# Performance work log

Measured on AMD Instinct MI355X. Metric: run time of the kernel, lower is better.

The kernel has to match this reference:

```python
import jax, jax.numpy as jnp
import numpy as np

B, A, D = 512, 32, 256      # batch clips, actors (nodes per graph), feature dim
E = 1048576                 # total edges over the flattened (B*A)-node graph
THRESHOLD = 0.5             # config.knn.threshold
EPS = 1e-5


def setup_inputs() -> dict:
    key = jax.random.key(0)
    k1, k2, k3 = jax.random.split(key, 3)
    N = B * A
    X = jax.random.normal(k1, (B, A, D), dtype=jnp.float32)
    edge_index = jax.random.randint(k2, (2, E), 0, N, dtype=jnp.int32)
    W = jax.random.normal(k3, (D, D), dtype=jnp.float32) * (1.0 / np.sqrt(D))
    b = jnp.zeros((D,), dtype=jnp.float32)
    return {"X": X, "edge_index": edge_index, "W": W, "b": b}


def gcn_conv(x, edge_index, W, b):
    # Standard GCNConv: x' = D^-1/2 (A + I) D^-1/2 (x W) + b
    N = x.shape[0]
    x = x @ W                                            # [N, D]
    loop = jnp.arange(N, dtype=edge_index.dtype)
    src = jnp.concatenate([edge_index[0], loop])         # message sources
    tgt = jnp.concatenate([edge_index[1], loop])         # aggregation targets
    deg = jax.ops.segment_sum(jnp.ones_like(src, dtype=x.dtype), tgt,
                              num_segments=N)            # in-degree incl. self-loop
    dinv = jnp.where(deg > 0, jax.lax.rsqrt(deg), 0.0)
    coef = (dinv[src] * dinv[tgt])[:, None]              # symmetric norm per edge
    out = jax.ops.segment_sum(x[src] * coef, tgt, num_segments=N)
    return out + b


def reference(X, edge_index, W, b):
    Bq, Aq, Dq = X.shape
    x = X.reshape(Bq * Aq, Dq)
    x = gcn_conv(x, edge_index, W, b)
    Xo = x.reshape(Bq, Aq, Dq)

    # cal_edge: pairwise squared distances per batch, min-max normalized,
    # thresholded. Instead of variable-length dense_to_sparse edge lists we
    # return the equivalent fixed-shape adjacency mask [B, A, A].
    inner = -2.0 * jnp.einsum('bad,bcd->bac', Xo, Xo)
    sq = jnp.sum(Xo * Xo, axis=-1, keepdims=True)        # [B, A, 1]
    scores = sq + inner + jnp.swapaxes(sq, -1, -2)       # [B, A, A]
    smin = scores.min(axis=-1, keepdims=True)
    smax = scores.max(axis=-1, keepdims=True)
    scores = (scores - smin) / (smax - smin + EPS)
    adj_mask = scores > THRESHOLD                        # new edge set (dense form)
    return Xo, adj_mask
```

## Files before the change

kernel.cpp:

```cpp
#include <hip/hip_runtime.h>

#define BQ 512
#define AQ 32
#define DQ 256
#define NQ (BQ * AQ)
#define EQ 1048576
#define THR 0.5f
#define EPSF 1e-5f
#define DEG_STRIDE 160
#define BIN_TGTS 64
#define NBINS (NQ / BIN_TGTS)
#define NBLK_P 256
#define EPB (EQ / NBLK_P)

typedef __attribute__((ext_vector_type(8))) short bf16x8;
typedef __attribute__((ext_vector_type(4))) float f32x4;

__device__ __forceinline__ unsigned short f2bf(float f) {
    unsigned int u = __float_as_uint(f);
    return (unsigned short)((u + 0x7FFFu + ((u >> 16) & 1u)) >> 16);
}
__device__ __forceinline__ float bf2f(unsigned short h) {
    return __uint_as_float((unsigned int)h << 16);
}

__global__ __launch_bounds__(256) void k_wt_part(
        const float* __restrict__ W, unsigned short* __restrict__ Wt,
        const int* __restrict__ src, const int* __restrict__ tgt,
        int* __restrict__ cntT, int* __restrict__ offT,
        unsigned int* __restrict__ binned) {
    __shared__ unsigned int buf[EPB];
    __shared__ int hist[NBINS];
    __shared__ int sdat[NBINS];
    __shared__ int cur[NBINS];
    int tid = threadIdx.x;
    if (blockIdx.x < 256) {
        int idx = blockIdx.x * 256 + tid;
        int n = idx >> 8;
        int k = idx & 255;
        float w = W[k * DQ + n];
        unsigned short h = f2bf(w);
        Wt[idx] = h;
        Wt[DQ * DQ + idx] = f2bf(w - bf2f(h));
        return;
    }
    int blk = blockIdx.x - 256;
    hist[tid] = 0;
    __syncthreads();
    int base = blk * EPB;
    int t[16], s[16];
    #pragma unroll
    for (int i = 0; i < 16; i++) {
        int e = base + i * 256 + tid;
        t[i] = tgt[e];
        s[i] = src[e];
        atomicAdd(&hist[t[i] >> 6], 1);
    }
    __syncthreads();
    int v = hist[tid];
    sdat[tid] = v;
    __syncthreads();
    #pragma unroll
    for (int off = 1; off < 256; off <<= 1) {
        int add = (tid >= off) ? sdat[tid - off] : 0;
        __syncthreads();
        sdat[tid] += add;
        __syncthreads();
    }
    int excl = sdat[tid] - v;
    cur[tid] = excl;
    cntT[blk * NBINS + tid] = v;
    offT[blk * NBINS + tid] = excl;
    __syncthreads();
    #pragma unroll
    for (int i = 0; i < 16; i++) {
        int pos = atomicAdd(&cur[t[i] >> 6], 1);
        buf[pos] = ((unsigned int)t[i] << 14) | (unsigned int)s[i];
    }
    __syncthreads();
    unsigned int* g = binned + (size_t)blk * EPB;
    #pragma unroll
    for (int i = 0; i < 16; i++) g[i * 256 + tid] = buf[i * 256 + tid];
}

__global__ __launch_bounds__(256) void k_gemm_cnt(
        const float* __restrict__ Xp, const unsigned short* __restrict__ Wt,
        unsigned short* __restrict__ xwb,
        const int* __restrict__ cntT, const int* __restrict__ offT,
        const unsigned int* __restrict__ binned,
        float* __restrict__ dinv) {
    __shared__ unsigned short bs[2][256 * 40];
    int tid = threadIdx.x;
    if (blockIdx.x >= 256) {
        int* lcnt = (int*)&bs[0][0];
        int b = blockIdx.x - 256;
        if (tid < BIN_TGTS) lcnt[tid] = 0;
        __syncthreads();
        int c = cntT[tid * NBINS + b];
        int o = offT[tid * NBINS + b];
        const unsigned int* e = binned + (size_t)tid * EPB + o;
        for (int j = 0; j < c; j++)
            atomicAdd(&lcnt[(e[j] >> 14) & 63], 1);
        __syncthreads();
        if (tid < BIN_TGTS)
            dinv[b * BIN_TGTS + tid] = rsqrtf((float)(lcnt[tid] + 1));
        return;
    }
    int wave = tid >> 6;
    int lane = tid & 63;
    int col = lane & 15;
    int quad = lane >> 4;
    int mbase = blockIdx.x * 64 + wave * 16;
    int m = mbase + col;

    const float* arow = Xp + (size_t)m * DQ;
    const unsigned short* Wlo = Wt + DQ * DQ;

    f32x4 acc[16];
    f32x4 zero = {0.f, 0.f, 0.f, 0.f};
    #pragma unroll
    for (int i = 0; i < 16; i++) acc[i] = zero;

    for (int k0 = 0; k0 < DQ; k0 += 32) {
        __syncthreads();
        {
            const uint4* gh = (const uint4*)(Wt + tid * DQ + k0);
            const uint4* gl = (const uint4*)(Wlo + tid * DQ + k0);
            uint4* lh = (uint4*)&bs[0][tid * 40];
            uint4* ll = (uint4*)&bs[1][tid * 40];
            #pragma unroll
            for (int u = 0; u < 4; u++) lh[u] = gh[u];
            #pragma unroll
            for (int u = 0; u < 4; u++) ll[u] = gl[u];
        }
        __syncthreads();

        int kq = k0 + quad * 8;
        float4 a0 = *(const float4*)(arow + kq);
        float4 a1 = *(const float4*)(arow + kq + 4);
        float av[8] = {a0.x, a0.y, a0.z, a0.w, a1.x, a1.y, a1.z, a1.w};
        bf16x8 ah, al;
        #pragma unroll
        for (int j = 0; j < 8; j++) {
            unsigned short h = f2bf(av[j]);
            ah[j] = (short)h;
            al[j] = (short)f2bf(av[j] - bf2f(h));
        }
        #pragma unroll
        for (int nt = 0; nt < 16; nt++) {
            int n = nt * 16 + col;
            bf16x8 bh = *(const bf16x8*)&bs[0][n * 40 + quad * 8];
            bf16x8 bl = *(const bf16x8*)&bs[1][n * 40 + quad * 8];
            acc[nt] = __builtin_amdgcn_mfma_f32_16x16x32_bf16(ah, bh, acc[nt], 0, 0, 0);
            acc[nt] = __builtin_amdgcn_mfma_f32_16x16x32_bf16(al, bh, acc[nt], 0, 0, 0);
            acc[nt] = __builtin_amdgcn_mfma_f32_16x16x32_bf16(ah, bl, acc[nt], 0, 0, 0);
        }
    }

    #pragma unroll
    for (int nt = 0; nt < 16; nt++) {
        #pragma unroll
        for (int r = 0; r < 4; r++) {
            xwb[(size_t)(mbase + quad * 4 + r) * DQ + nt * 16 + col] =
                f2bf(acc[nt][r]);
        }
    }
}

__global__ __launch_bounds__(512) void k_agg_scores(
        const unsigned int* __restrict__ xwb,
        const unsigned int* __restrict__ binned,
        const int* __restrict__ cntT, const int* __restrict__ offT,
        const float* __restrict__ dinv,
        const float* __restrict__ bias,
        float* __restrict__ out,
        float* __restrict__ mask) {
    __shared__ float xs[AQ][DQ + 4];
    __shared__ float sq[AQ];
    __shared__ float sc[AQ][AQ + 1];
    __shared__ float rmin[AQ], rmax[AQ];
    __shared__ unsigned short lbuck[AQ * DEG_STRIDE];
    __shared__ int lcnt[AQ];

    int tid = threadIdx.x;
    int wave = tid >> 6;
    int lane = tid & 63;
    int bq = blockIdx.x;
    const uint2* xw2 = (const uint2*)xwb;

    if (tid < AQ) lcnt[tid] = 0;
    __syncthreads();
    {
        int b = bq >> 1;
        int blk = tid & 255;
        int half = tid >> 8;
        int c = cntT[blk * NBINS + b];
        int o = offT[blk * NBINS + b];
        const unsigned int* ebase = binned + (size_t)blk * EPB + o;
        for (int j = half; j < c; j += 2) {
            unsigned int ed = ebase[j];
            if ((int)(ed >> 19) == bq) {
                int a = (ed >> 14) & 31;
                int pos = atomicAdd(&lcnt[a], 1);
                if (pos < DEG_STRIDE)
                    lbuck[a * DEG_STRIDE + pos] = (unsigned short)(ed & 0x3FFFu);
            }
        }
    }
    __syncthreads();

    float4 bv = ((const float4*)bias)[lane];

    #pragma unroll 1
    for (int i = 0; i < 4; i++) {
        int a = wave * 4 + i;
        int t = bq * AQ + a;
        float dt = dinv[t];
        float c0 = dt * dt;
        uint2 sp = xw2[(size_t)t * 64 + lane];
        float4 acc;
        acc.x = __uint_as_float(sp.x << 16) * c0;
        acc.y = __uint_as_float(sp.x & 0xFFFF0000u) * c0;
        acc.z = __uint_as_float(sp.y << 16) * c0;
        acc.w = __uint_as_float(sp.y & 0xFFFF0000u) * c0;

        int num = lcnt[a];
        if (num > DEG_STRIDE) num = DEG_STRIDE;
        for (int k0 = 0; k0 < num; k0 += 64) {
            int rem = num - k0;
            int n = rem < 64 ? rem : 64;
            int idx = k0 + (lane < n ? lane : 0);
            int e = (int)lbuck[a * DEG_STRIDE + idx];
            float cl = (lane < n) ? dinv[e] * dt : 0.f;
            int n8 = (n + 7) & ~7;
            for (int j0 = 0; j0 < n8; j0 += 8) {
                #pragma unroll
                for (int jj = 0; jj < 8; jj++) {
                    int j = j0 + jj;
                    int s = __shfl(e, j);
                    float c = __shfl(cl, j);
                    uint2 p = xw2[(size_t)s * 64 + lane];
                    acc.x += __uint_as_float(p.x << 16) * c;
                    acc.y += __uint_as_float(p.x & 0xFFFF0000u) * c;
                    acc.z += __uint_as_float(p.y << 16) * c;
                    acc.w += __uint_as_float(p.y & 0xFFFF0000u) * c;
                }
            }
        }

        acc.x += bv.x; acc.y += bv.y; acc.z += bv.z; acc.w += bv.w;
        ((float4*)out)[(size_t)t * 64 + lane] = acc;
        *(float4*)&xs[a][lane * 4] = acc;
    }
    __syncthreads();

    if (tid < AQ) {
        const float4* xi = (const float4*)xs[tid];
        float s = 0.f;
        #pragma unroll 8
        for (int dd = 0; dd < DQ / 4; dd++) {
            float4 a = xi[dd];
            s += a.x * a.x + a.y * a.y + a.z * a.z + a.w * a.w;
        }
        sq[tid] = s;
    }
    __syncthreads();

    {
        int p0 = tid * 2;
        int i = p0 >> 5;
        int j0 = p0 & 31;
        const float4* xi = (const float4*)xs[i];
        float g[2] = {0.f, 0.f};
        for (int dd = 0; dd < DQ / 4; dd += 8) {
            float4 ar[8];
            #pragma unroll
            for (int u = 0; u < 8; u++) ar[u] = xi[dd + u];
            #pragma unroll
            for (int q = 0; q < 2; q++) {
                const float4* xj = (const float4*)xs[j0 + q];
                float gq = 0.f;
                #pragma unroll
                for (int u = 0; u < 8; u++) {
                    float4 b = xj[dd + u];
                    gq += ar[u].x * b.x + ar[u].y * b.y +
                          ar[u].z * b.z + ar[u].w * b.w;
                }
                g[q] += gq;
            }
        }
        #pragma unroll
        for (int q = 0; q < 2; q++) {
            sc[i][j0 + q] = sq[i] - 2.f * g[q] + sq[j0 + q];
        }
    }
    __syncthreads();

    if (tid < AQ) {
        float mn = sc[tid][0], mx = sc[tid][0];
        for (int j = 1; j < AQ; j++) {
            float v = sc[tid][j];
            mn = fminf(mn, v);
            mx = fmaxf(mx, v);
        }
        rmin[tid] = mn;
        rmax[tid] = mx;
    }
    __syncthreads();

    {
        float* mb = mask + (size_t)bq * AQ * AQ;
        int p0 = tid * 2;
        int i = p0 >> 5, j0 = p0 & 31;
        float inv = 1.0f / (rmax[i] - rmin[i] + EPSF);
        float2 mv;
        mv.x = ((sc[i][j0 + 0] - rmin[i]) * inv > THR) ? 1.0f : 0.0f;
        mv.y = ((sc[i][j0 + 1] - rmin[i]) * inv > THR) ? 1.0f : 0.0f;
        ((float2*)mb)[tid] = mv;
    }
}

extern "C" void kernel_launch(void* const* d_in, const int* in_sizes, int n_in,
                              void* d_out, int out_size, void* d_ws, size_t ws_size,
                              hipStream_t stream) {
    const float* X    = (const float*)d_in[0];
    const int*   ei   = (const int*)d_in[1];
    const float* W    = (const float*)d_in[2];
    const float* bias = (const float*)d_in[3];
    float* out = (float*)d_out;

    char* ws = (char*)d_ws;
    unsigned short* xwb = (unsigned short*)ws;
    unsigned int* binned = (unsigned int*)(ws + (size_t)NQ * DQ * 2);
    unsigned short* Wt = (unsigned short*)(binned + (size_t)NBLK_P * EPB);
    float* dinv = (float*)(Wt + 2 * DQ * DQ);
    int* cntT = (int*)(dinv + NQ);
    int* offT = cntT + NBLK_P * NBINS;

    const int* src = ei;
    const int* tgt = ei + EQ;

    k_wt_part<<<512, 256, 0, stream>>>(W, Wt, src, tgt, cntT, offT, binned);
    k_gemm_cnt<<<512, 256, 0, stream>>>(X, Wt, xwb, cntT, offT, binned, dinv);
    k_agg_scores<<<BQ, 512, 0, stream>>>((const unsigned int*)xwb, binned,
                                         cntT, offT, dinv, bias, out,
                                         out + (size_t)NQ * DQ);
}
```

Measured before the change: 174.2 us.

## Build per-target edge buckets in degree blocks instead of rescanning bins in aggregation

The degree-counting blocks of the GEMM kernel now also scatter source indices into per-target buckets in shared memory and write the buckets and counts to global memory. The aggregation kernel reads these buckets directly instead of rescanning every partition's bin and filtering by batch. This removes the redundant double scan of each bin (two batches share a bin) and the shared-memory bucketing work from the aggregation kernel. In exchange it adds a global write and read of the bucket array (NQ*160 shorts), and the reads of bucket rows and counts now go through global memory instead of LDS.

```diff
diff --git a/kernel.cpp b/kernel.cpp
--- a/kernel.cpp
+++ b/kernel.cpp
@@ -83,27 +83,41 @@
     for (int i = 0; i < 16; i++) g[i * 256 + tid] = buf[i * 256 + tid];
 }
 
-__global__ __launch_bounds__(256) void k_gemm_cnt(
+__global__ __launch_bounds__(256) void k_gemm_bucket(
         const float* __restrict__ Xp, const unsigned short* __restrict__ Wt,
         unsigned short* __restrict__ xwb,
         const int* __restrict__ cntT, const int* __restrict__ offT,
         const unsigned int* __restrict__ binned,
+        unsigned short* __restrict__ bucket, int* __restrict__ cnt,
         float* __restrict__ dinv) {
     __shared__ unsigned short bs[2][256 * 40];
+    __shared__ int lcnt[BIN_TGTS];
     int tid = threadIdx.x;
     if (blockIdx.x >= 256) {
-        int* lcnt = (int*)&bs[0][0];
+        unsigned short* lbuck = &bs[0][0];
         int b = blockIdx.x - 256;
         if (tid < BIN_TGTS) lcnt[tid] = 0;
         __syncthreads();
         int c = cntT[tid * NBINS + b];
         int o = offT[tid * NBINS + b];
         const unsigned int* e = binned + (size_t)tid * EPB + o;
-        for (int j = 0; j < c; j++)
-            atomicAdd(&lcnt[(e[j] >> 14) & 63], 1);
-        __syncthreads();
-        if (tid < BIN_TGTS)
-            dinv[b * BIN_TGTS + tid] = rsqrtf((float)(lcnt[tid] + 1));
+        for (int j = 0; j < c; j++) {
+            unsigned int ed = e[j];
+            int tl = (int)(ed >> 14) & 63;
+            int pos = atomicAdd(&lcnt[tl], 1);
+            if (pos < DEG_STRIDE)
+                lbuck[tl * DEG_STRIDE + pos] = (unsigned short)(ed & 0x3FFFu);
+        }
+        __syncthreads();
+        const unsigned int* lb32 = (const unsigned int*)lbuck;
+        unsigned int* gb32 = (unsigned int*)(bucket + (size_t)b * BIN_TGTS * DEG_STRIDE);
+        #pragma unroll
+        for (int i = 0; i < 20; i++) gb32[i * 256 + tid] = lb32[i * 256 + tid];
+        if (tid < BIN_TGTS) {
+            int cc = lcnt[tid];
+            cnt[b * BIN_TGTS + tid] = cc;
+            dinv[b * BIN_TGTS + tid] = rsqrtf((float)(cc + 1));
+        }
         return;
     }
     int wave = tid >> 6;
@@ -169,8 +183,8 @@
 
 __global__ __launch_bounds__(512) void k_agg_scores(
         const unsigned int* __restrict__ xwb,
-        const unsigned int* __restrict__ binned,
-        const int* __restrict__ cntT, const int* __restrict__ offT,
+        const int* __restrict__ cnt,
+        const unsigned short* __restrict__ bucket,
         const float* __restrict__ dinv,
         const float* __restrict__ bias,
         float* __restrict__ out,
@@ -179,35 +193,12 @@
     __shared__ float sq[AQ];
     __shared__ float sc[AQ][AQ + 1];
     __shared__ float rmin[AQ], rmax[AQ];
-    __shared__ unsigned short lbuck[AQ * DEG_STRIDE];
-    __shared__ int lcnt[AQ];
 
     int tid = threadIdx.x;
     int wave = tid >> 6;
     int lane = tid & 63;
     int bq = blockIdx.x;
     const uint2* xw2 = (const uint2*)xwb;
-
-    if (tid < AQ) lcnt[tid] = 0;
-    __syncthreads();
-    {
-        int b = bq >> 1;
-        int blk = tid & 255;
-        int half = tid >> 8;
-        int c = cntT[blk * NBINS + b];
-        int o = offT[blk * NBINS + b];
-        const unsigned int* ebase = binned + (size_t)blk * EPB + o;
-        for (int j = half; j < c; j += 2) {
-            unsigned int ed = ebase[j];
-            if ((int)(ed >> 19) == bq) {
-                int a = (ed >> 14) & 31;
-                int pos = atomicAdd(&lcnt[a], 1);
-                if (pos < DEG_STRIDE)
-                    lbuck[a * DEG_STRIDE + pos] = (unsigned short)(ed & 0x3FFFu);
-            }
-        }
-    }
-    __syncthreads();
 
     float4 bv = ((const float4*)bias)[lane];
 
@@ -224,13 +215,14 @@
         acc.z = __uint_as_float(sp.y << 16) * c0;
         acc.w = __uint_as_float(sp.y & 0xFFFF0000u) * c0;
 
-        int num = lcnt[a];
+        const unsigned short* brow = bucket + (size_t)t * DEG_STRIDE;
+        int num = cnt[t];
         if (num > DEG_STRIDE) num = DEG_STRIDE;
         for (int k0 = 0; k0 < num; k0 += 64) {
             int rem = num - k0;
             int n = rem < 64 ? rem : 64;
             int idx = k0 + (lane < n ? lane : 0);
-            int e = (int)lbuck[a * DEG_STRIDE + idx];
+            int e = (int)brow[idx];
             float cl = (lane < n) ? dinv[e] * dt : 0.f;
             int n8 = (n + 7) & ~7;
             for (int j0 = 0; j0 < n8; j0 += 8) {
@@ -332,17 +324,20 @@
     char* ws = (char*)d_ws;
     unsigned short* xwb = (unsigned short*)ws;
     unsigned int* binned = (unsigned int*)(ws + (size_t)NQ * DQ * 2);
-    unsigned short* Wt = (unsigned short*)(binned + (size_t)NBLK_P * EPB);
+    unsigned short* bucket = (unsigned short*)(binned + (size_t)NBLK_P * EPB);
+    unsigned short* Wt = bucket + (size_t)NQ * DEG_STRIDE;
     float* dinv = (float*)(Wt + 2 * DQ * DQ);
-    int* cntT = (int*)(dinv + NQ);
+    int* cnt = (int*)(dinv + NQ);
+    int* cntT = cnt + NQ;
     int* offT = cntT + NBLK_P * NBINS;
 
     const int* src = ei;
     const int* tgt = ei + EQ;
 
     k_wt_part<<<512, 256, 0, stream>>>(W, Wt, src, tgt, cntT, offT, binned);
-    k_gemm_cnt<<<512, 256, 0, stream>>>(X, Wt, xwb, cntT, offT, binned, dinv);
-    k_agg_scores<<<BQ, 512, 0, stream>>>((const unsigned int*)xwb, binned,
-                                         cntT, offT, dinv, bias, out,
+    k_gemm_bucket<<<512, 256, 0, stream>>>(X, Wt, xwb, cntT, offT, binned,
+                                           bucket, cnt, dinv);
+    k_agg_scores<<<BQ, 512, 0, stream>>>((const unsigned int*)xwb, cnt, bucket,
+                                         dinv, bias, out,
                                          out + (size_t)NQ * DQ);
 }
```

Result: faster. 163.6 us, median of 2 (-6.1%).
